# Kernel tuning notes

Measured on AMD Instinct MI355X. Metric: run time of the kernel, lower is better.

The kernel has to match this reference:

```python
import math
import jax, jax.numpy as jnp
import numpy as np

DIM = 512; DEPTH = 12; HEADS = 8; DIM_HEAD = 64
INNER = HEADS * DIM_HEAD
FF_INNER = 4 * DIM
B = 8192
NUM_TIMESTEPS = 1000
SCALE = 16.0  # cosine_sim_scale
ROT_DIM = 32  # RotaryEmbedding(dim=min(32, dim_head))
NUM_BUCKETS = 32; MAX_DISTANCE = 128


def layer_norm(x, g, eps=1e-5):
    mean = jnp.mean(x, axis=-1, keepdims=True)
    var = jnp.mean((x - mean) ** 2, axis=-1, keepdims=True)  # unbiased=False
    return (x - mean) * jax.lax.rsqrt(var + eps) * g


def l2norm(t):
    n = jnp.linalg.norm(t, axis=-1, keepdims=True)
    return t / jnp.maximum(n, 1e-12)


def rotary_freqs(n):
    inv = 1.0 / (10000.0 ** (jnp.arange(0, ROT_DIM, 2, dtype=jnp.float32) / ROT_DIM))
    f = jnp.arange(n, dtype=jnp.float32)[:, None] * inv[None, :]  # (n, ROT_DIM//2)
    return jnp.repeat(f, 2, axis=-1)  # (n, ROT_DIM), interleaved pairs


def rotate_half(x):
    x1 = x[..., 0::2]; x2 = x[..., 1::2]
    return jnp.stack((-x2, x1), axis=-1).reshape(x.shape)


def apply_rotary(t, freqs):
    tr, tp = t[..., :ROT_DIM], t[..., ROT_DIM:]
    tr = tr * jnp.cos(freqs) + rotate_half(tr) * jnp.sin(freqs)
    return jnp.concatenate([tr, tp], axis=-1)


def rel_pos_bias(i, j, emb):
    rel = jnp.arange(j)[None, :] - jnp.arange(i)[:, None]
    n = jnp.maximum(-rel, 0)
    max_exact = NUM_BUCKETS // 2
    nf = jnp.maximum(n, 1).astype(jnp.float32)
    val_large = max_exact + (jnp.log(nf / max_exact) / math.log(MAX_DISTANCE / max_exact) * (NUM_BUCKETS - max_exact)).astype(jnp.int32)
    val_large = jnp.minimum(val_large, NUM_BUCKETS - 1)
    bucket = jnp.where(n < max_exact, n, val_large)
    return emb[bucket].transpose(2, 0, 1)  # (h, i, j)


def setup_inputs() -> dict:
    key = jax.random.key(0)
    ks = jax.random.split(key, 13)
    w = 0.02
    return {
        "image_embed": jax.random.normal(ks[0], (B, DIM), jnp.float32),
        "text_embed": jax.random.normal(ks[1], (B, DIM), jnp.float32),
        "timesteps": jax.random.randint(ks[2], (B,), 0, NUM_TIMESTEPS),
        "time_emb_table": jax.random.normal(ks[3], (NUM_TIMESTEPS, DIM)) * w,
        "learned_query": jax.random.normal(ks[4], (DIM,)),
        "rel_emb": jax.random.normal(ks[5], (NUM_BUCKETS, HEADS)) * w,
        "attn_norm_g": jnp.ones((DEPTH, DIM)),
        "Wq": jax.random.normal(ks[6], (DEPTH, DIM, INNER)) * w,
        "Wkv": jax.random.normal(ks[7], (DEPTH, DIM, 2 * DIM_HEAD)) * w,
        "null_kv": jax.random.normal(ks[8], (DEPTH, 2, DIM_HEAD)),
        "Wo": jax.random.normal(ks[9], (DEPTH, INNER, DIM)) * w,
        "attn_out_norm_g": jnp.ones((DEPTH, DIM)),
        "ff_norm_g": jnp.ones((DEPTH, DIM)),
        "Wff1": jax.random.normal(ks[10], (DEPTH, DIM, 2 * FF_INNER)) * w,
        "Wff2": jax.random.normal(ks[11], (DEPTH, FF_INNER, DIM)) * w,
        "final_norm_g": jnp.ones((DIM,)),
        "Wproj": jax.random.normal(ks[12], (DIM, DIM)) * w,
    }


def reference(image_embed, text_embed, timesteps, time_emb_table, learned_query, rel_emb,
              attn_norm_g, Wq, Wkv, null_kv, Wo, attn_out_norm_g,
              ff_norm_g, Wff1, Wff2, final_norm_g, Wproj):
    b = image_embed.shape[0]
    # token sequence: [text_embed, time_embed, image_embed, learned_query] -> (b, 4, dim)
    tokens = jnp.concatenate([
        text_embed[:, None, :],
        time_emb_table[timesteps][:, None, :],
        image_embed[:, None, :],
        jnp.broadcast_to(learned_query, (b, 1, DIM)),
    ], axis=1)
    n = tokens.shape[1]
    bias = rel_pos_bias(n, n + 1, rel_emb)            # (h, n, n+1)
    freqs = rotary_freqs(n)                           # (n, ROT_DIM)
    causal = jnp.triu(jnp.ones((n, n + 1), dtype=bool), k=2)
    neg = -jnp.finfo(jnp.float32).max
    sqrt_scale = math.sqrt(SCALE)

    x = tokens
    for l in range(DEPTH):
        # --- Attention ---
        h = layer_norm(x, attn_norm_g[l])
        q = (h @ Wq[l]).reshape(b, n, HEADS, DIM_HEAD).transpose(0, 2, 1, 3) * SCALE
        kv = h @ Wkv[l]
        k, v = kv[..., :DIM_HEAD], kv[..., DIM_HEAD:]  # single-head kv (b, n, d)
        q = apply_rotary(q, freqs)
        k = apply_rotary(k, freqs)
        nk = jnp.broadcast_to(null_kv[l, 0], (b, 1, DIM_HEAD))
        nv = jnp.broadcast_to(null_kv[l, 1], (b, 1, DIM_HEAD))
        k = jnp.concatenate([nk, k], axis=1)
        v = jnp.concatenate([nv, v], axis=1)
        q = l2norm(q) * sqrt_scale
        k = l2norm(k) * sqrt_scale
        sim = jnp.einsum('bhid,bjd->bhij', q, k) + bias[None]
        sim = jnp.where(causal[None, None], neg, sim)
        attn = jax.nn.softmax(sim.astype(jnp.float32), axis=-1).astype(sim.dtype)
        out = jnp.einsum('bhij,bjd->bhid', attn, v).transpose(0, 2, 1, 3).reshape(b, n, INNER)
        x = x + layer_norm(out @ Wo[l], attn_out_norm_g[l])
        # --- SwiGLU FFN ---
        h = layer_norm(x, ff_norm_g[l])
        hg = h @ Wff1[l]
        a, g = hg[..., :FF_INNER], hg[..., FF_INNER:]
        x = x + (a * jax.nn.silu(g)) @ Wff2[l]

    x = layer_norm(x, final_norm_g) @ Wproj
    return x[:, -1, :]  # predicted image embed from learned query position
```

## Files before the change

kernel.cpp:

```cpp
#include <hip/hip_runtime.h>

typedef __bf16 bf16x8 __attribute__((ext_vector_type(8)));
typedef __bf16 bf16x4 __attribute__((ext_vector_type(4)));
typedef __bf16 bf16x2 __attribute__((ext_vector_type(2)));
typedef float  f32x4  __attribute__((ext_vector_type(4)));
typedef unsigned short u16;

#define BATCH   8192
#define NTOK    4
#define ROWS    (BATCH*NTOK)
#define DIM     512
#define HEADS   8
#define DH      64
#define FFI     2048
#define DEPTH   12
#define LN_EPS  1e-5f

static const size_t OFF_WQKV = 0;
static const size_t SZ_WQKV  = 12ull*640*512*2;
static const size_t OFF_WTO  = OFF_WQKV + SZ_WQKV;
static const size_t SZ_WTO   = 12ull*512*512*2;
static const size_t OFF_WTF1 = OFF_WTO + SZ_WTO;
static const size_t SZ_WTF1  = 12ull*4096*512*2;
static const size_t OFF_WTF2 = OFF_WTF1 + SZ_WTF1;
static const size_t SZ_WTF2  = 12ull*512*2048*2;
static const size_t OFF_WTP  = OFF_WTF2 + SZ_WTF2;
static const size_t SZ_WTP   = 512ull*512*2;
static const size_t OFF_X    = OFF_WTP + SZ_WTP;
static const size_t OFF_H    = OFF_X    + (size_t)ROWS*DIM*4;
static const size_t OFF_QKV  = OFF_H    + (size_t)ROWS*DIM*2;
static const size_t OFF_AO   = OFF_QKV  + (size_t)ROWS*640*2;
static const size_t OFF_FLAG = OFF_AO   + (size_t)ROWS*DIM*2;
static const size_t WS_NEED  = OFF_FLAG + 256;

__device__ __forceinline__ float ldf(const void* p, size_t i, bool b16) {
  return b16 ? (float)((const __bf16*)p)[i] : ((const float*)p)[i];
}

__device__ __forceinline__ void gld_lds16(const void* g, void* l) {
  __builtin_amdgcn_global_load_lds((const __attribute__((address_space(1))) void*)g,
                                   (__attribute__((address_space(3))) void*)l, 16, 0, 0);
}

__device__ __forceinline__ float gsum16(float v) {
  #pragma unroll
  for (int o = 8; o > 0; o >>= 1) v += __shfl_xor(v, o, 64);
  return v;
}

__device__ __forceinline__ void wred2(float& a, float& b) {
  #pragma unroll
  for (int o = 32; o > 0; o >>= 1) { a += __shfl_xor(a, o, 64); b += __shfl_xor(b, o, 64); }
}

__global__ void detect_dtype(const unsigned int* __restrict__ w, int* __restrict__ flag) {
  __shared__ int cnt[4];
  int t = threadIdx.x;
  int c = 0;
  for (int i = t; i < 2048; i += 256) {
    unsigned int v = w[i];
    unsigned int lo = v & 0xFFFFu, hi = v >> 16;
    int elo = (int)((lo >> 7) & 0xFF), ehi = (int)((hi >> 7) & 0xFF);
    bool okl = (lo == 0u) || (elo >= 100 && elo <= 140);
    bool okh = (hi == 0u) || (ehi >= 100 && ehi <= 140);
    if (okl && okh) c++;
  }
  #pragma unroll
  for (int o = 32; o > 0; o >>= 1) c += __shfl_down(c, o, 64);
  if ((t & 63) == 0) cnt[t >> 6] = c;
  __syncthreads();
  if (t == 0) flag[0] = (cnt[0] + cnt[1] + cnt[2] + cnt[3] > 1024) ? 1 : 0;
}

__global__ void transpose_any(const void* __restrict__ in, u16* __restrict__ out,
                              int K, int N, size_t out_zsz, int rowoff, int mode,
                              const int* __restrict__ flag) {
  bool b16 = flag[0] != 0;
  __shared__ u16 tile[32][33];
  size_t iboff = (size_t)blockIdx.z * K * N;
  size_t oboff = (size_t)blockIdx.z * out_zsz;
  int n0 = blockIdx.x * 32, k0 = blockIdx.y * 32;
  int tx = threadIdx.x, ty = threadIdx.y;
  #pragma unroll
  for (int r = 0; r < 4; r++) {
    float v = ldf(in, iboff + (size_t)(k0 + ty*4 + r) * N + n0 + tx, b16);
    __bf16 bv = (__bf16)v;
    tile[ty*4+r][tx] = __builtin_bit_cast(u16, bv);
  }
  __syncthreads();
  int rbase;
  if (mode == 0) rbase = rowoff + n0;
  else {
    int s = (n0 >= 2048) ? 1 : 0;
    int np = n0 - s*2048;
    rbase = (np >> 7)*256 + ((np >> 5) & 3)*64 + s*32;
  }
  #pragma unroll
  for (int r = 0; r < 4; r++)
    out[oboff + (size_t)(rbase + ty*4 + r) * K + k0 + tx] = tile[tx][ty*4+r];
}

__global__ void build_tokens(const void* __restrict__ text, const void* __restrict__ img,
                             const int* __restrict__ ts, const void* __restrict__ table,
                             const void* __restrict__ lq, float* __restrict__ x,
                             const int* __restrict__ flag) {
  bool b16 = flag[0] != 0;
  int b = blockIdx.x, t = threadIdx.x;
  float* xr = x + (size_t)b * NTOK * DIM;
  int tsb = ts[b];
  for (int e = t; e < DIM; e += 256) {
    xr[e]         = ldf(text,  (size_t)b * DIM + e, b16);
    xr[DIM + e]   = ldf(table, (size_t)tsb * DIM + e, b16);
    xr[2*DIM + e] = ldf(img,   (size_t)b * DIM + e, b16);
    xr[3*DIM + e] = ldf(lq,    (size_t)e, b16);
  }
}

__global__ void ln_f32_bf16(const float* __restrict__ x, const void* __restrict__ g, size_t goff,
                            __bf16* __restrict__ out, const int* __restrict__ flag) {
  bool b16 = flag[0] != 0;
  int lane = threadIdx.x & 63;
  int row = blockIdx.x * 4 + (threadIdx.x >> 6);
  const float4* xr = (const float4*)(x + (size_t)row * DIM);
  float4 A4 = xr[lane*2], B4 = xr[lane*2 + 1];
  float v[8] = {A4.x, A4.y, A4.z, A4.w, B4.x, B4.y, B4.z, B4.w};
  float s = 0.f, s2 = 0.f;
  #pragma unroll
  for (int e = 0; e < 8; e++) { s += v[e]; s2 += v[e]*v[e]; }
  wred2(s, s2);
  float mean = s * (1.f/DIM);
  float var  = s2 * (1.f/DIM) - mean*mean;
  float rs = rsqrtf(var + LN_EPS);
  bf16x8 ov;
  #pragma unroll
  for (int e = 0; e < 8; e++)
    ov[e] = (__bf16)((v[e]-mean) * rs * ldf(g, goff + lane*8 + e, b16));
  *(bf16x8*)(out + (size_t)row * DIM + lane*8) = ov;
}

__global__ void ln_add_ln(const __bf16* __restrict__ y,
                          const void* __restrict__ g1, size_t g1off,
                          const void* __restrict__ g2, size_t g2off,
                          float* __restrict__ x, __bf16* __restrict__ h,
                          const int* __restrict__ flag) {
  bool b16 = flag[0] != 0;
  int lane = threadIdx.x & 63;
  int row = blockIdx.x * 4 + (threadIdx.x >> 6);
  bf16x8 y8 = *(const bf16x8*)(y + (size_t)row * DIM + lane*8);
  float yv[8];
  float s = 0.f, s2 = 0.f;
  #pragma unroll
  for (int e = 0; e < 8; e++) { yv[e] = (float)y8[e]; s += yv[e]; s2 += yv[e]*yv[e]; }
  wred2(s, s2);
  float mean = s * (1.f/DIM);
  float var  = s2 * (1.f/DIM) - mean*mean;
  float rs = rsqrtf(var + LN_EPS);
  float4* xr = (float4*)(x + (size_t)row * DIM);
  float4 XA = xr[lane*2], XB = xr[lane*2 + 1];
  float xv[8] = {XA.x, XA.y, XA.z, XA.w, XB.x, XB.y, XB.z, XB.w};
  #pragma unroll
  for (int e = 0; e < 8; e++)
    xv[e] += (yv[e]-mean) * rs * ldf(g1, g1off + lane*8 + e, b16);
  xr[lane*2]     = make_float4(xv[0], xv[1], xv[2], xv[3]);
  xr[lane*2 + 1] = make_float4(xv[4], xv[5], xv[6], xv[7]);
  float t = 0.f, t2 = 0.f;
  #pragma unroll
  for (int e = 0; e < 8; e++) { t += xv[e]; t2 += xv[e]*xv[e]; }
  wred2(t, t2);
  float mean2 = t * (1.f/DIM);
  float var2  = t2 * (1.f/DIM) - mean2*mean2;
  float rs2 = rsqrtf(var2 + LN_EPS);
  bf16x8 hv;
  #pragma unroll
  for (int e = 0; e < 8; e++)
    hv[e] = (__bf16)((xv[e]-mean2) * rs2 * ldf(g2, g2off + lane*8 + e, b16));
  *(bf16x8*)(h + (size_t)row * DIM + lane*8) = hv;
}

__global__ void ln_final(const float* __restrict__ x, const void* __restrict__ g,
                         __bf16* __restrict__ out, const int* __restrict__ flag) {
  bool b16 = flag[0] != 0;
  int lane = threadIdx.x & 63;
  int b = blockIdx.x * 4 + (threadIdx.x >> 6);
  int row = b*NTOK + 3;
  const float4* xr = (const float4*)(x + (size_t)row * DIM);
  float4 A4 = xr[lane*2], B4 = xr[lane*2 + 1];
  float v[8] = {A4.x, A4.y, A4.z, A4.w, B4.x, B4.y, B4.z, B4.w};
  float s = 0.f, s2 = 0.f;
  #pragma unroll
  for (int e = 0; e < 8; e++) { s += v[e]; s2 += v[e]*v[e]; }
  wred2(s, s2);
  float mean = s * (1.f/DIM);
  float var  = s2 * (1.f/DIM) - mean*mean;
  float rs = rsqrtf(var + LN_EPS);
  bf16x8 ov;
  #pragma unroll
  for (int e = 0; e < 8; e++)
    ov[e] = (__bf16)((v[e]-mean) * rs * ldf(g, (size_t)lane*8 + e, b16));
  *(bf16x8*)(out + (size_t)b * DIM + lane*8) = ov;
}

template<int BROWS, int EPI>
__global__ __launch_bounds__(512, 2) void gemm8(
    const __bf16* __restrict__ A, int lda,
    const __bf16* __restrict__ B, int ldb,
    void* __restrict__ Cv, int ldc, int K, const int* __restrict__ flag)
{
  constexpr int UNITS = (BROWS == 256) ? 4 : 3;
  constexpr int WCN   = (BROWS == 256) ? 4 : 2;
  constexpr int M_FR  = (BROWS == 256) ? 8 : 4;
  __shared__ char ldsmem[2][(256 + BROWS) * 128];

  const int tid = threadIdx.x;
  const int wid = tid >> 6, lane = tid & 63;
  const int wr = wid / WCN, wc = wid % WCN;
  const int lr = lane & 15, lc = lane >> 4;
  const int sr = tid >> 3;
  const int cs = ((tid & 7) ^ (sr & 7)) * 8;
  const int bx = blockIdx.x, by = blockIdx.y;

  const __bf16* Ab = A + (size_t)by * 256 * lda;
  const __bf16* Bb = B + (size_t)bx * BROWS * ldb;

  f32x4 acc[M_FR][4] = {};
  const int NT = K >> 6;

  char* lds0 = ldsmem[0];
  char* lds1 = ldsmem[1];

  auto stage_unit = [&](char* base, int kt, int u) {
    if (u < 2) {
      const __bf16* s = Ab + (size_t)(u*128 + sr) * lda + kt*64 + cs;
      char* d = base + u*16384 + (wid << 10);
      gld_lds16(s, d);
      gld_lds16(s + (size_t)64 * lda, d + 8192);
    } else {
      const __bf16* s = Bb + (size_t)((u-2)*128 + sr) * ldb + kt*64 + cs;
      char* d = base + 32768 + (u-2)*16384 + (wid << 10);
      gld_lds16(s, d);
      gld_lds16(s + (size_t)64 * ldb, d + 8192);
    }
  };

  #pragma unroll
  for (int u = 0; u < UNITS; u++) stage_unit(lds0, 0, u);

  for (int t = 0; t < NT; t++) {
    char* cbase = (t & 1) ? lds1 : lds0;
    char* sbase = (t & 1) ? lds0 : lds1;
    const int st = (t + 1 < NT) ? (t + 1) : 0;
    #pragma unroll
    for (int u = 0; u < UNITS; u++) stage_unit(sbase, st, u);
    asm volatile("s_waitcnt vmcnt(%0)" :: "i"(2*UNITS) : "memory");
    asm volatile("s_barrier" ::: "memory");
    bf16x8 bfr[4][2];
    #pragma unroll
    for (int f = 0; f < 4; f++)
      #pragma unroll
      for (int kk = 0; kk < 2; kk++) {
        int row = wc*64 + f*16 + lr;
        int ch = (kk*4 + lc) ^ (lr & 7);
        bfr[f][kk] = *(const bf16x8*)(cbase + 32768 + row*128 + ch*16);
      }
    __builtin_amdgcn_s_setprio(1);
    #pragma unroll
    for (int m = 0; m < M_FR; m++) {
      bf16x8 afr[2];
      #pragma unroll
      for (int kk = 0; kk < 2; kk++) {
        int row = wr*(M_FR*16) + m*16 + lr;
        int ch = (kk*4 + lc) ^ (lr & 7);
        afr[kk] = *(const bf16x8*)(cbase + row*128 + ch*16);
      }
      #pragma unroll
      for (int n = 0; n < 4; n++)
        #pragma unroll
        for (int kk = 0; kk < 2; kk++)
          acc[m][n] = __builtin_amdgcn_mfma_f32_16x16x32_bf16(
              afr[kk], bfr[n][kk], acc[m][n], 0, 0, 0);
    }
    __builtin_amdgcn_s_setprio(0);
    asm volatile("s_barrier" ::: "memory");
  }
  asm volatile("s_waitcnt vmcnt(0)" ::: "memory");

  if (EPI == 1) {
    __bf16* Ob = (__bf16*)Cv;
    const int colb = bx*128 + wc*32 + lr;
    const int rowb = by*256 + wr*128 + lc*4;
    #pragma unroll
    for (int m = 0; m < M_FR; m++)
      #pragma unroll
      for (int rr = 0; rr < 4; rr++) {
        size_t ro = (size_t)(rowb + m*16 + rr) * ldc;
        #pragma unroll
        for (int fa = 0; fa < 2; fa++) {
          float a = acc[m][fa][rr], g = acc[m][fa+2][rr];
          Ob[ro + colb + fa*16] = (__bf16)(a * g / (1.f + __expf(-g)));
        }
      }
  } else if (EPI == 2) {
    float* Xf = (float*)Cv;
    const int colb = bx*BROWS + wc*64 + lr;
    const int rowb = by*256 + wr*(M_FR*16) + lc*4;
    #pragma unroll
    for (int m = 0; m < M_FR; m++)
      #pragma unroll
      for (int rr = 0; rr < 4; rr++) {
        size_t ro = (size_t)(rowb + m*16 + rr) * ldc;
        #pragma unroll
        for (int n = 0; n < 4; n++) Xf[ro + colb + n*16] += acc[m][n][rr];
      }
  } else if (EPI == 0) {
    __bf16* Cb = (__bf16*)Cv;
    const int colb = bx*BROWS + wc*64 + lr;
    const int rowb = by*256 + wr*(M_FR*16) + lc*4;
    #pragma unroll
    for (int m = 0; m < M_FR; m++)
      #pragma unroll
      for (int rr = 0; rr < 4; rr++) {
        size_t ro = (size_t)(rowb + m*16 + rr) * ldc;
        #pragma unroll
        for (int n = 0; n < 4; n++) Cb[ro + colb + n*16] = (__bf16)acc[m][n][rr];
      }
  } else {
    bool b16o = flag[0] != 0;
    __bf16* Cb = (__bf16*)Cv;
    float*  Cf = (float*)Cv;
    const int colb = bx*BROWS + wc*64 + lr;
    const int rowb = by*256 + wr*(M_FR*16) + lc*4;
    #pragma unroll
    for (int m = 0; m < M_FR; m++)
      #pragma unroll
      for (int rr = 0; rr < 4; rr++) {
        size_t ro = (size_t)(rowb + m*16 + rr) * ldc;
        #pragma unroll
        for (int n = 0; n < 4; n++) {
          float val = acc[m][n][rr];
          if (b16o) Cb[ro + colb + n*16] = (__bf16)val; else Cf[ro + colb + n*16] = val;
        }
      }
  }
}

__global__ __launch_bounds__(256) void attn_kernel(
    const __bf16* __restrict__ qkv,
    const void* __restrict__ nkv_all, int layer, const void* __restrict__ rel_emb,
    __bf16* __restrict__ ao, const int* __restrict__ flag)
{
  bool b16 = flag[0] != 0;
  const int tid = threadIdx.x;
  const int w = tid >> 6, l = tid & 63;
  const int g = l >> 4, c = l & 15;
  const int bh = blockIdx.x * 16 + w * 4 + g;
  const int b = bh >> 3, h = bh & 7;
  const bool rot = (c < 8);

  const float LN1E4_32 = 9.210340371976184f * (1.f/32.f);
  float inv0 = __expf(-(float)(4*c)     * LN1E4_32);
  float inv1 = __expf(-(float)(4*c + 2) * LN1E4_32);
  float cs0[4], sn0[4], cs1[4], sn1[4];
  #pragma unroll
  for (int t = 0; t < 4; t++) {
    __sincosf((float)t * inv0, &sn0[t], &cs0[t]);
    __sincosf((float)t * inv1, &sn1[t], &cs1[t]);
  }
  float rb[4];
  #pragma unroll
  for (int t = 0; t < 4; t++) rb[t] = ldf(rel_emb, (size_t)t * 8 + h, b16);

  float q[4][4];
  #pragma unroll
  for (int i = 0; i < 4; i++) {
    bf16x4 qv = *(const bf16x4*)(qkv + ((size_t)(b*NTOK + i)) * 640 + h*DH + c*4);
    float v0 = (float)qv[0], v1 = (float)qv[1], v2 = (float)qv[2], v3 = (float)qv[3];
    if (rot) {
      float n0 = v0*cs0[i] - v1*sn0[i], n1 = v1*cs0[i] + v0*sn0[i];
      float n2 = v2*cs1[i] - v3*sn1[i], n3 = v3*cs1[i] + v2*sn1[i];
      v0 = n0; v1 = n1; v2 = n2; v3 = n3;
    }
    q[i][0] = v0; q[i][1] = v1; q[i][2] = v2; q[i][3] = v3;
  }
  #pragma unroll
  for (int i = 0; i < 4; i++) {
    float ss = q[i][0]*q[i][0] + q[i][1]*q[i][1] + q[i][2]*q[i][2] + q[i][3]*q[i][3];
    float r = 1.f / fmaxf(sqrtf(gsum16(ss)), 1e-12f);
    #pragma unroll
    for (int e = 0; e < 4; e++) q[i][e] *= r;
  }

  float kk[5][4], vv[5][4];
  #pragma unroll
  for (int e = 0; e < 4; e++) {
    kk[0][e] = ldf(nkv_all, (size_t)layer*128 + c*4 + e, b16);
    vv[0][e] = ldf(nkv_all, (size_t)layer*128 + 64 + c*4 + e, b16);
  }
  #pragma unroll
  for (int j = 1; j < 5; j++) {
    const __bf16* base = qkv + ((size_t)(b*NTOK + j - 1)) * 640 + 512;
    bf16x4 kv4 = *(const bf16x4*)(base + c*4);
    bf16x4 vv4 = *(const bf16x4*)(base + 64 + c*4);
    float v0 = (float)kv4[0], v1 = (float)kv4[1], v2 = (float)kv4[2], v3 = (float)kv4[3];
    if (rot) {
      int t = j - 1;
      float n0 = v0*cs0[t] - v1*sn0[t], n1 = v1*cs0[t] + v0*sn0[t];
      float n2 = v2*cs1[t] - v3*sn1[t], n3 = v3*cs1[t] + v2*sn1[t];
      v0 = n0; v1 = n1; v2 = n2; v3 = n3;
    }
    kk[j][0] = v0; kk[j][1] = v1; kk[j][2] = v2; kk[j][3] = v3;
    #pragma unroll
    for (int e = 0; e < 4; e++) vv[j][e] = (float)vv4[e];
  }
  #pragma unroll
  for (int j = 0; j < 5; j++) {
    float ss = kk[j][0]*kk[j][0] + kk[j][1]*kk[j][1] + kk[j][2]*kk[j][2] + kk[j][3]*kk[j][3];
    float r = 1.f / fmaxf(sqrtf(gsum16(ss)), 1e-12f);
    #pragma unroll
    for (int e = 0; e < 4; e++) kk[j][e] *= r;
  }

  #pragma unroll
  for (int i = 0; i < 4; i++) {
    float sim[5];
    #pragma unroll
    for (int j = 0; j < 5; j++) {
      if (j > i + 1) break;
      float pp = q[i][0]*kk[j][0] + q[i][1]*kk[j][1] + q[i][2]*kk[j][2] + q[i][3]*kk[j][3];
      sim[j] = 16.f * gsum16(pp) + rb[(i - j > 0) ? (i - j) : 0];
    }
    float m = sim[0];
    #pragma unroll
    for (int j = 1; j < 5; j++) { if (j > i + 1) break; m = fmaxf(m, sim[j]); }
    float Z = 0.f, o0 = 0.f, o1 = 0.f, o2 = 0.f, o3 = 0.f;
    #pragma unroll
    for (int j = 0; j < 5; j++) {
      if (j > i + 1) break;
      float e = __expf(sim[j] - m);
      Z += e;
      o0 += e * vv[j][0]; o1 += e * vv[j][1]; o2 += e * vv[j][2]; o3 += e * vv[j][3];
    }
    float rz = 1.f / Z;
    bf16x4 ov = { (__bf16)(o0*rz), (__bf16)(o1*rz), (__bf16)(o2*rz), (__bf16)(o3*rz) };
    *(bf16x4*)(ao + ((size_t)(b*NTOK + i)) * DIM + h*DH + c*4) = ov;
  }
}

extern "C" void kernel_launch(void* const* d_in, const int* in_sizes, int n_in,
                              void* d_out, int out_size, void* d_ws, size_t ws_size,
                              hipStream_t stream) {
  const void* image_embed     = d_in[0];
  const void* text_embed      = d_in[1];
  const int*  timesteps       = (const int*)d_in[2];
  const void* time_table      = d_in[3];
  const void* learned_query   = d_in[4];
  const void* rel_emb         = d_in[5];
  const void* attn_norm_g     = d_in[6];
  const void* Wq              = d_in[7];
  const void* Wkv             = d_in[8];
  const void* null_kv         = d_in[9];
  const void* Wo              = d_in[10];
  const void* attn_out_norm_g = d_in[11];
  const void* ff_norm_g       = d_in[12];
  const void* Wff1            = d_in[13];
  const void* Wff2            = d_in[14];
  const void* final_norm_g    = d_in[15];
  const void* Wproj           = d_in[16];

  if (ws_size < WS_NEED) return;

  char* ws = (char*)d_ws;
  __bf16* wqkv = (__bf16*)(ws + OFF_WQKV);
  __bf16* wto  = (__bf16*)(ws + OFF_WTO);
  __bf16* wtf1 = (__bf16*)(ws + OFF_WTF1);
  __bf16* wtf2 = (__bf16*)(ws + OFF_WTF2);
  __bf16* wtp  = (__bf16*)(ws + OFF_WTP);
  float*  x    = (float*) (ws + OFF_X);
  __bf16* h    = (__bf16*)(ws + OFF_H);
  __bf16* qkv  = (__bf16*)(ws + OFF_QKV);
  __bf16* ao   = (__bf16*)(ws + OFF_AO);
  __bf16* act  = (__bf16*)(ws + OFF_QKV);
  int*    flag = (int*)   (ws + OFF_FLAG);

  detect_dtype<<<1, 256, 0, stream>>>((const unsigned int*)Wq, flag);

  dim3 tb(32, 8);
  transpose_any<<<dim3(16, 16, 12),  tb, 0, stream>>>(Wq,   (u16*)wqkv, 512,  512,  640ull*512, 0,   0, flag);
  transpose_any<<<dim3(4,  16, 12),  tb, 0, stream>>>(Wkv,  (u16*)wqkv, 512,  128,  640ull*512, 512, 0, flag);
  transpose_any<<<dim3(16, 16, 12),  tb, 0, stream>>>(Wo,   (u16*)wto,  512,  512,  512ull*512, 0,   0, flag);
  transpose_any<<<dim3(128,16, 12),  tb, 0, stream>>>(Wff1, (u16*)wtf1, 512,  4096, 4096ull*512,0,   1, flag);
  transpose_any<<<dim3(16, 64, 12),  tb, 0, stream>>>(Wff2, (u16*)wtf2, 2048, 512,  512ull*2048,0,   0, flag);
  transpose_any<<<dim3(16, 16, 1),   tb, 0, stream>>>(Wproj,(u16*)wtp,  512,  512,  512ull*512, 0,   0, flag);

  build_tokens<<<BATCH, 256, 0, stream>>>(text_embed, image_embed, timesteps, time_table,
                                          learned_query, x, flag);

  for (int l = 0; l < DEPTH; l++) {
    const __bf16* wqkv_l = wqkv + (size_t)l * 640 * 512;
    const __bf16* wto_l  = wto  + (size_t)l * 512 * 512;
    const __bf16* wtf1_l = wtf1 + (size_t)l * 4096 * 512;
    const __bf16* wtf2_l = wtf2 + (size_t)l * 512 * 2048;

    ln_f32_bf16<<<ROWS/4, 256, 0, stream>>>(x, attn_norm_g, (size_t)l*DIM, h, flag);
    gemm8<128,0><<<dim3(5, 128), 512, 0, stream>>>(h, DIM, wqkv_l, 512, qkv, 640, 512, flag);
    attn_kernel<<<BATCH/2, 256, 0, stream>>>(qkv, null_kv, l, rel_emb, ao, flag);
    gemm8<128,0><<<dim3(4, 128), 512, 0, stream>>>(ao, DIM, wto_l, 512, qkv , DIM, 512, flag);
    ln_add_ln<<<ROWS/4, 256, 0, stream>>>(qkv , attn_out_norm_g, (size_t)l*DIM,
                                          ff_norm_g, (size_t)l*DIM, x, h, flag);

    for (int c = 0; c < 2; c++) {
      const __bf16* hc = h + (size_t)c * 16384 * DIM;
      float*        xc = x + (size_t)c * 16384 * DIM;
      gemm8<256,1><<<dim3(16, 64), 512, 0, stream>>>(hc, DIM, wtf1_l, 512, act, FFI, 512, flag);
      gemm8<128,2><<<dim3(4, 64), 512, 0, stream>>>(act, FFI, wtf2_l, FFI, xc, DIM, 2048, flag);
    }
  }

  ln_final<<<BATCH/4, 256, 0, stream>>>(x, final_norm_g, ao , flag);
  gemm8<128,3><<<dim3(4, 32), 512, 0, stream>>>(ao, DIM, wtp, 512, d_out, DIM, 512, flag);
}
```

Baseline: 5.809 ms.

## Add 128x128 GEMM kernel and interleave staging with MFMA quarters in gemm8

Adds a new 256-thread gemm128 kernel with 128x128 tiles for the QKV, output-projection, FF2 and final projection GEMMs. This doubles the block count for better CU occupancy and load balance. The gemm8 main loop, still used for FF1, is unrolled by two and split into four quarters, with one global-to-LDS staging unit issued before each quarter's MFMAs to overlap loads with compute. The cost is more barriers per tile and lower per-block reuse in the smaller tiles. The loop now assumes K/64 is even.

```diff
diff --git a/kernel.cpp b/kernel.cpp
--- a/kernel.cpp
+++ b/kernel.cpp
@@ -209,6 +209,7 @@
   constexpr int UNITS = (BROWS == 256) ? 4 : 3;
   constexpr int WCN   = (BROWS == 256) ? 4 : 2;
   constexpr int M_FR  = (BROWS == 256) ? 8 : 4;
+  constexpr int QM    = M_FR / 4;
   __shared__ char ldsmem[2][(256 + BROWS) * 128];
 
   const int tid = threadIdx.x;
@@ -228,7 +229,8 @@
   char* lds0 = ldsmem[0];
   char* lds1 = ldsmem[1];
 
-  auto stage_unit = [&](char* base, int kt, int u) {
+  auto stage_unit = [&](int p, int kt, int u) {
+    char* base = (p ? lds1 : lds0);
     if (u < 2) {
       const __bf16* s = Ab + (size_t)(u*128 + sr) * lda + kt*64 + cs;
       char* d = base + u*16384 + (wid << 10);
@@ -243,44 +245,55 @@
   };
 
   #pragma unroll
-  for (int u = 0; u < UNITS; u++) stage_unit(lds0, 0, u);
-
-  for (int t = 0; t < NT; t++) {
-    char* cbase = (t & 1) ? lds1 : lds0;
-    char* sbase = (t & 1) ? lds0 : lds1;
-    const int st = (t + 1 < NT) ? (t + 1) : 0;
-    #pragma unroll
-    for (int u = 0; u < UNITS; u++) stage_unit(sbase, st, u);
-    asm volatile("s_waitcnt vmcnt(%0)" :: "i"(2*UNITS) : "memory");
-    asm volatile("s_barrier" ::: "memory");
-    bf16x8 bfr[4][2];
-    #pragma unroll
-    for (int f = 0; f < 4; f++)
-      #pragma unroll
-      for (int kk = 0; kk < 2; kk++) {
-        int row = wc*64 + f*16 + lr;
-        int ch = (kk*4 + lc) ^ (lr & 7);
-        bfr[f][kk] = *(const bf16x8*)(cbase + 32768 + row*128 + ch*16);
-      }
-    __builtin_amdgcn_s_setprio(1);
-    #pragma unroll
-    for (int m = 0; m < M_FR; m++) {
-      bf16x8 afr[2];
-      #pragma unroll
-      for (int kk = 0; kk < 2; kk++) {
-        int row = wr*(M_FR*16) + m*16 + lr;
-        int ch = (kk*4 + lc) ^ (lr & 7);
-        afr[kk] = *(const bf16x8*)(cbase + row*128 + ch*16);
-      }
-      #pragma unroll
-      for (int n = 0; n < 4; n++)
-        #pragma unroll
-        for (int kk = 0; kk < 2; kk++)
-          acc[m][n] = __builtin_amdgcn_mfma_f32_16x16x32_bf16(
-              afr[kk], bfr[n][kk], acc[m][n], 0, 0, 0);
-    }
-    __builtin_amdgcn_s_setprio(0);
-    asm volatile("s_barrier" ::: "memory");
+  for (int u = 0; u < UNITS; u++) stage_unit(0, 0, u);
+
+  const int NIT = NT >> 1;
+  for (int i = 0; i < NIT; i++) {
+    const int t1 = 2*i + 1;
+    const int t2 = (2*i + 2 < NT) ? (2*i + 2) : 0;
+    #pragma unroll
+    for (int hfl = 0; hfl < 2; hfl++) {
+      char* cbase = hfl ? lds1 : lds0;
+      const int sp = hfl ^ 1;
+      const int st = hfl ? t2 : t1;
+      bf16x8 bfr[4][2];
+      #pragma unroll
+      for (int q = 0; q < 4; q++) {
+        if (q < UNITS) stage_unit(sp, st, q);
+        if (q == 0) {
+          asm volatile("s_waitcnt vmcnt(2)" ::: "memory");
+          asm volatile("s_barrier" ::: "memory");
+          #pragma unroll
+          for (int f = 0; f < 4; f++)
+            #pragma unroll
+            for (int kk = 0; kk < 2; kk++) {
+              int row = wc*64 + f*16 + lr;
+              int ch = (kk*4 + lc) ^ (lr & 7);
+              bfr[f][kk] = *(const bf16x8*)(cbase + 32768 + row*128 + ch*16);
+            }
+        }
+        bf16x8 afr[QM][2];
+        #pragma unroll
+        for (int m2 = 0; m2 < QM; m2++)
+          #pragma unroll
+          for (int kk = 0; kk < 2; kk++) {
+            int row = wr*(M_FR*16) + (q*QM + m2)*16 + lr;
+            int ch = (kk*4 + lc) ^ (lr & 7);
+            afr[m2][kk] = *(const bf16x8*)(cbase + row*128 + ch*16);
+          }
+        __builtin_amdgcn_s_setprio(1);
+        #pragma unroll
+        for (int m2 = 0; m2 < QM; m2++)
+          #pragma unroll
+          for (int n = 0; n < 4; n++)
+            #pragma unroll
+            for (int kk = 0; kk < 2; kk++)
+              acc[q*QM + m2][n] = __builtin_amdgcn_mfma_f32_16x16x32_bf16(
+                  afr[m2][kk], bfr[n][kk], acc[q*QM + m2][n], 0, 0, 0);
+        __builtin_amdgcn_s_setprio(0);
+        asm volatile("s_barrier" ::: "memory");
+      }
+    }
   }
   asm volatile("s_waitcnt vmcnt(0)" ::: "memory");
 
@@ -299,24 +312,103 @@
           Ob[ro + colb + fa*16] = (__bf16)(a * g / (1.f + __expf(-g)));
         }
       }
-  } else if (EPI == 2) {
-    float* Xf = (float*)Cv;
-    const int colb = bx*BROWS + wc*64 + lr;
-    const int rowb = by*256 + wr*(M_FR*16) + lc*4;
-    #pragma unroll
-    for (int m = 0; m < M_FR; m++)
-      #pragma unroll
-      for (int rr = 0; rr < 4; rr++) {
-        size_t ro = (size_t)(rowb + m*16 + rr) * ldc;
-        #pragma unroll
-        for (int n = 0; n < 4; n++) Xf[ro + colb + n*16] += acc[m][n][rr];
-      }
-  } else if (EPI == 0) {
+  } else {
     __bf16* Cb = (__bf16*)Cv;
     const int colb = bx*BROWS + wc*64 + lr;
     const int rowb = by*256 + wr*(M_FR*16) + lc*4;
     #pragma unroll
     for (int m = 0; m < M_FR; m++)
+      #pragma unroll
+      for (int rr = 0; rr < 4; rr++) {
+        size_t ro = (size_t)(rowb + m*16 + rr) * ldc;
+        #pragma unroll
+        for (int n = 0; n < 4; n++) Cb[ro + colb + n*16] = (__bf16)acc[m][n][rr];
+      }
+  }
+}
+
+template<int EPI>
+__global__ __launch_bounds__(256, 2) void gemm128(
+    const __bf16* __restrict__ A, int lda,
+    const __bf16* __restrict__ B, int ldb,
+    void* __restrict__ Cv, int ldc, int K, const int* __restrict__ flag)
+{
+  __shared__ char ldsmem[2][32768];
+  const int tid = threadIdx.x;
+  const int wid = tid >> 6, lane = tid & 63;
+  const int wr = wid >> 1, wc = wid & 1;
+  const int lr = lane & 15, lc = lane >> 4;
+  const int bx = blockIdx.x, by = blockIdx.y;
+  const __bf16* Ab = A + (size_t)by * 128 * lda;
+  const __bf16* Bb = B + (size_t)bx * 128 * ldb;
+  f32x4 acc[4][4] = {};
+  const int NT = K >> 6;
+
+  const int rg0 = (wid << 3) + (lane >> 3);
+  const int scol = ((lane & 7) ^ (rg0 & 7)) * 8;
+
+  auto stage = [&](char* base, int kt) {
+    #pragma unroll
+    for (int r = 0; r < 4; r++) {
+      gld_lds16(Ab + (size_t)(r*32 + rg0)*lda + kt*64 + scol, base + r*4096 + (wid << 10));
+      gld_lds16(Bb + (size_t)(r*32 + rg0)*ldb + kt*64 + scol, base + 16384 + r*4096 + (wid << 10));
+    }
+  };
+
+  stage(ldsmem[0], 0);
+  for (int t = 0; t < NT; t++) {
+    char* cbase = ldsmem[t & 1];
+    char* sbase = ldsmem[(t & 1) ^ 1];
+    stage(sbase, (t + 1 < NT) ? (t + 1) : 0);
+    asm volatile("s_waitcnt vmcnt(8)" ::: "memory");
+    asm volatile("s_barrier" ::: "memory");
+    bf16x8 bfr[4][2];
+    #pragma unroll
+    for (int f = 0; f < 4; f++)
+      #pragma unroll
+      for (int kk = 0; kk < 2; kk++) {
+        int row = wc*64 + f*16 + lr;
+        int ch = (kk*4 + lc) ^ (lr & 7);
+        bfr[f][kk] = *(const bf16x8*)(cbase + 16384 + row*128 + ch*16);
+      }
+    __builtin_amdgcn_s_setprio(1);
+    #pragma unroll
+    for (int m = 0; m < 4; m++) {
+      bf16x8 afr[2];
+      #pragma unroll
+      for (int kk = 0; kk < 2; kk++) {
+        int row = wr*64 + m*16 + lr;
+        int ch = (kk*4 + lc) ^ (lr & 7);
+        afr[kk] = *(const bf16x8*)(cbase + row*128 + ch*16);
+      }
+      #pragma unroll
+      for (int n = 0; n < 4; n++)
+        #pragma unroll
+        for (int kk = 0; kk < 2; kk++)
+          acc[m][n] = __builtin_amdgcn_mfma_f32_16x16x32_bf16(
+              afr[kk], bfr[n][kk], acc[m][n], 0, 0, 0);
+    }
+    __builtin_amdgcn_s_setprio(0);
+    asm volatile("s_barrier" ::: "memory");
+  }
+  asm volatile("s_waitcnt vmcnt(0)" ::: "memory");
+
+  const int colb = bx*128 + wc*64 + lr;
+  const int rowb = by*128 + wr*64 + lc*4;
+  if (EPI == 2) {
+    float* Xf = (float*)Cv;
+    #pragma unroll
+    for (int m = 0; m < 4; m++)
+      #pragma unroll
+      for (int rr = 0; rr < 4; rr++) {
+        size_t ro = (size_t)(rowb + m*16 + rr) * ldc;
+        #pragma unroll
+        for (int n = 0; n < 4; n++) Xf[ro + colb + n*16] += acc[m][n][rr];
+      }
+  } else if (EPI == 0) {
+    __bf16* Cb = (__bf16*)Cv;
+    #pragma unroll
+    for (int m = 0; m < 4; m++)
       #pragma unroll
       for (int rr = 0; rr < 4; rr++) {
         size_t ro = (size_t)(rowb + m*16 + rr) * ldc;
@@ -327,10 +419,8 @@
     bool b16o = flag[0] != 0;
     __bf16* Cb = (__bf16*)Cv;
     float*  Cf = (float*)Cv;
-    const int colb = bx*BROWS + wc*64 + lr;
-    const int rowb = by*256 + wr*(M_FR*16) + lc*4;
-    #pragma unroll
-    for (int m = 0; m < M_FR; m++)
+    #pragma unroll
+    for (int m = 0; m < 4; m++)
       #pragma unroll
       for (int rr = 0; rr < 4; rr++) {
         size_t ro = (size_t)(rowb + m*16 + rr) * ldc;
@@ -501,9 +591,9 @@
     const __bf16* wtf2_l = wtf2 + (size_t)l * 512 * 2048;
 
     ln_f32_bf16<<<ROWS/4, 256, 0, stream>>>(x, attn_norm_g, (size_t)l*DIM, h, flag);
-    gemm8<128,0><<<dim3(5, 128), 512, 0, stream>>>(h, DIM, wqkv_l, 512, qkv, 640, 512, flag);
+    gemm128<0><<<dim3(5, 256), 256, 0, stream>>>(h, DIM, wqkv_l, 512, qkv, 640, 512, flag);
     attn_kernel<<<BATCH/2, 256, 0, stream>>>(qkv, null_kv, l, rel_emb, ao, flag);
-    gemm8<128,0><<<dim3(4, 128), 512, 0, stream>>>(ao, DIM, wto_l, 512, qkv , DIM, 512, flag);
+    gemm128<0><<<dim3(4, 256), 256, 0, stream>>>(ao, DIM, wto_l, 512, qkv , DIM, 512, flag);
     ln_add_ln<<<ROWS/4, 256, 0, stream>>>(qkv , attn_out_norm_g, (size_t)l*DIM,
                                           ff_norm_g, (size_t)l*DIM, x, h, flag);
 
@@ -511,10 +601,10 @@
       const __bf16* hc = h + (size_t)c * 16384 * DIM;
       float*        xc = x + (size_t)c * 16384 * DIM;
       gemm8<256,1><<<dim3(16, 64), 512, 0, stream>>>(hc, DIM, wtf1_l, 512, act, FFI, 512, flag);
-      gemm8<128,2><<<dim3(4, 64), 512, 0, stream>>>(act, FFI, wtf2_l, FFI, xc, DIM, 2048, flag);
+      gemm128<2><<<dim3(4, 128), 256, 0, stream>>>(act, FFI, wtf2_l, FFI, xc, DIM, 2048, flag);
     }
   }
 
   ln_final<<<BATCH/4, 256, 0, stream>>>(x, final_norm_g, ao , flag);
-  gemm8<128,3><<<dim3(4, 32), 512, 0, stream>>>(ao, DIM, wtp, 512, d_out, DIM, 512, flag);
-}
+  gemm128<3><<<dim3(4, 64), 256, 0, stream>>>(ao, DIM, wtp, 512, d_out, DIM, 512, flag);
+}
```

New measurement: 5.661 ms. 2.5% less time.
